# Performance work log

Hardware: AMD Instinct MI355X
Metric: run time of the kernel (lower is better)

The kernel has to match this reference:

```python
import jax, jax.numpy as jnp
import numpy as np

NUM_FEATURES = 602
NUM_CLASSES = 41
HIDDEN = 8
HEADS1 = 8
HEADS2 = 1
N_NODES = 100000
N_EDGES = 1600000
NEG_SLOPE = 0.2  # PyG GATConv default leaky_relu slope
EPS = 1e-16      # PyG softmax denominator epsilon


def gat_conv(x, edge_index, W, att_src, att_dst, bias, heads, out_ch, concat):
    """Faithful PyG GATConv forward (eval mode, dropout disabled).
    x: [N, F_in], edge_index: [2, E] with row0=src, row1=dst.
    W: [F_in, heads*out_ch], att_src/att_dst: [heads, out_ch], bias: [heads*out_ch] or [out_ch].
    """
    N = x.shape[0]
    h = (x @ W).reshape(N, heads, out_ch)              # [N, H, C]
    a_src = jnp.einsum('nhc,hc->nh', h, att_src)       # [N, H]
    a_dst = jnp.einsum('nhc,hc->nh', h, att_dst)       # [N, H]
    src, dst = edge_index[0], edge_index[1]
    e = jax.nn.leaky_relu(a_src[src] + a_dst[dst], NEG_SLOPE)  # [E, H]
    # segment softmax over incoming edges of each dst node
    m = jax.ops.segment_max(e, dst, num_segments=N)    # [N, H]
    e = jnp.exp(e - m[dst])
    denom = jax.ops.segment_sum(e, dst, num_segments=N)  # [N, H]
    alpha = e / (denom[dst] + EPS)                     # [E, H]
    msg = h[src] * alpha[:, :, None]                   # [E, H, C]
    out = jax.ops.segment_sum(msg, dst, num_segments=N)  # [N, H, C]
    if concat:
        out = out.reshape(N, heads * out_ch)
    else:
        out = out.mean(axis=1)
    return out + bias


def setup_inputs() -> dict:
    key = jax.random.key(0)
    ks = jax.random.split(key, 10)
    x = jax.random.normal(ks[0], (N_NODES, NUM_FEATURES), dtype=jnp.float32)
    edge_index = jax.random.randint(ks[1], (2, N_EDGES), 0, N_NODES, dtype=jnp.int64)
    s = 0.1
    W1 = jax.random.normal(ks[2], (NUM_FEATURES, HEADS1 * HIDDEN), dtype=jnp.float32) * s
    att_src1 = jax.random.normal(ks[3], (HEADS1, HIDDEN), dtype=jnp.float32) * s
    att_dst1 = jax.random.normal(ks[4], (HEADS1, HIDDEN), dtype=jnp.float32) * s
    b1 = jnp.zeros((HEADS1 * HIDDEN,), dtype=jnp.float32)
    W2 = jax.random.normal(ks[5], (HEADS1 * HIDDEN, HEADS2 * NUM_CLASSES), dtype=jnp.float32) * s
    att_src2 = jax.random.normal(ks[6], (HEADS2, NUM_CLASSES), dtype=jnp.float32) * s
    att_dst2 = jax.random.normal(ks[7], (HEADS2, NUM_CLASSES), dtype=jnp.float32) * s
    b2 = jnp.zeros((NUM_CLASSES,), dtype=jnp.float32)
    return {"x": x, "edge_index": edge_index, "W1": W1, "att_src1": att_src1,
            "att_dst1": att_dst1, "b1": b1, "W2": W2, "att_src2": att_src2,
            "att_dst2": att_dst2, "b2": b2}


def reference(x, edge_index, W1, att_src1, att_dst1, b1, W2, att_src2, att_dst2, b2):
    # eval mode: all F.dropout calls are identity
    h = gat_conv(x, edge_index, W1, att_src1, att_dst1, b1, HEADS1, HIDDEN, concat=True)
    h = jax.nn.elu(h)
    h = gat_conv(h, edge_index, W2, att_src2, att_dst2, b2, HEADS2, NUM_CLASSES, concat=False)
    return jax.nn.log_softmax(h, axis=1)
```

## Files before the change

kernel.cpp:

```cpp
#include <hip/hip_runtime.h>
#include <math.h>

#define NN 100000
#define NE 1600000
#define F_IN 602
#define H1 8
#define C1 8
#define F_MID 64
#define NC 41
#define NEG_SLOPE 0.2f
#define WT_LD 640

#define LRELU(x) fmaxf((x), NEG_SLOPE * (x))

typedef __attribute__((ext_vector_type(8))) short short8;
typedef __attribute__((ext_vector_type(4))) float f32x4;

__device__ inline unsigned short f2bf(float f) {
    unsigned u = __builtin_bit_cast(unsigned, f);
    unsigned r = (u + 0x7FFFu + ((u >> 16) & 1u)) >> 16;
    return (unsigned short)r;
}

__global__ void zero_kernel(int4* __restrict__ p, int n4)
{
    int i = blockIdx.x * blockDim.x + threadIdx.x;
    if (i < n4) p[i] = make_int4(0, 0, 0, 0);
}

__global__ void prep_wt_kernel(const float* __restrict__ W, unsigned short* __restrict__ Wt)
{
    int idx = blockIdx.x * blockDim.x + threadIdx.x;
    if (idx >= F_MID * WT_LD) return;
    int col = idx / WT_LD, k = idx % WT_LD;
    Wt[idx] = (k < F_IN) ? f2bf(W[k * F_MID + col]) : (unsigned short)0;
}

__global__ __launch_bounds__(256) void gemm1_mfma(
    const float* __restrict__ x, const unsigned short* __restrict__ Wt,
    float* __restrict__ h, int N)
{
    __shared__ unsigned short As[64][40];
    __shared__ unsigned short Bs[64][40];

    int t = threadIdx.x;
    int lane = t & 63;
    int w = t >> 6;
    int l16 = lane & 15, lg = lane >> 4;
    int n0 = blockIdx.x * 64;

    int arow = t >> 2, aseg = t & 3;
    int grow = n0 + arow;
    const float* xrow = x + (size_t)(grow < N ? grow : 0) * F_IN + aseg * 8;
    int bcol = t >> 2;
    const unsigned short* wrow = Wt + (size_t)bcol * WT_LD + aseg * 8;

    f32x4 acc[4] = {};
    float2 av[4];
    uint4  bv;

    #pragma unroll
    for (int i = 0; i < 4; ++i) av[i] = *(const float2*)(xrow + i * 2);
    bv = *(const uint4*)(wrow);

    for (int kt = 0; kt < 19; ++kt) {
        __syncthreads();
        {
            unsigned short tmp[8];
            #pragma unroll
            for (int i = 0; i < 4; ++i) {
                tmp[i * 2]     = f2bf(av[i].x);
                tmp[i * 2 + 1] = f2bf(av[i].y);
            }
            *(uint4*)(&As[arow][aseg * 8]) = *(uint4*)tmp;
            *(uint4*)(&Bs[bcol][aseg * 8]) = bv;
        }
        __syncthreads();

        if (kt < 18) {
            int k0 = (kt + 1) * 32;
            if (kt + 1 < 18) {
                #pragma unroll
                for (int i = 0; i < 4; ++i) av[i] = *(const float2*)(xrow + k0 + i * 2);
            } else {
                #pragma unroll
                for (int i = 0; i < 4; ++i) {
                    int k = k0 + aseg * 8 + i * 2;
                    float a = (k < F_IN)     ? xrow[k0 + i * 2]     : 0.f;
                    float b = (k + 1 < F_IN) ? xrow[k0 + i * 2 + 1] : 0.f;
                    av[i] = make_float2(a, b);
                }
            }
            bv = *(const uint4*)(wrow + k0);
        }

        short8 afrag = *(const short8*)(&As[w * 16 + l16][lg * 8]);
        short8 bfrag[4];
        #pragma unroll
        for (int n = 0; n < 4; ++n)
            bfrag[n] = *(const short8*)(&Bs[n * 16 + l16][lg * 8]);
        #pragma unroll
        for (int n = 0; n < 4; ++n)
            acc[n] = __builtin_amdgcn_mfma_f32_16x16x32_bf16(afrag, bfrag[n], acc[n], 0, 0, 0);
    }

    #pragma unroll
    for (int r = 0; r < 4; ++r) {
        int row = n0 + w * 16 + lg * 4 + r;
        if (row < N) {
            #pragma unroll
            for (int n = 0; n < 4; ++n)
                h[(size_t)row * F_MID + n * 16 + l16] = acc[n][r];
        }
    }
}

__global__ void attn1_kernel(const float* __restrict__ h,
                             const float* __restrict__ attS,
                             const float* __restrict__ attD,
                             float* __restrict__ asrc, float* __restrict__ adst, int N)
{
    int idx = blockIdx.x * blockDim.x + threadIdx.x;
    if (idx >= N * H1) return;
    int n = idx >> 3, hh = idx & 7;
    float s = 0.f, d = 0.f;
    #pragma unroll
    for (int c = 0; c < C1; ++c) {
        float v = h[n * F_MID + hh * C1 + c];
        s += v * attS[hh * C1 + c];
        d += v * attD[hh * C1 + c];
    }
    asrc[idx] = s;
    adst[idx] = d;
}

__global__ void deg_kernel(const int* __restrict__ dst, int* __restrict__ deg, int E)
{
    int e = blockIdx.x * blockDim.x + threadIdx.x;
    if (e < E) atomicAdd(&deg[dst[e]], 1);
}

__global__ void scan1_kernel(const int* __restrict__ deg, int* __restrict__ bsum, int N)
{
    int b = blockIdx.x, t = threadIdx.x;
    int base = b * 1024 + t * 16;
    int s = 0;
    #pragma unroll
    for (int i = 0; i < 16; ++i) { int idx = base + i; if (idx < N) s += deg[idx]; }
    #pragma unroll
    for (int o = 32; o > 0; o >>= 1) s += __shfl_down(s, o);
    if (t == 0) bsum[b] = s;
}

__global__ void scan2_kernel(const int* __restrict__ bsum, int* __restrict__ boff,
                             int nb, int* __restrict__ offs, int N, int E)
{
    __shared__ int buf[128];
    int t = threadIdx.x;
    int v = (t < nb) ? bsum[t] : 0;
    buf[t] = v;
    __syncthreads();
    for (int o = 1; o < 128; o <<= 1) {
        int u = (t >= o) ? buf[t - o] : 0;
        __syncthreads();
        buf[t] += u;
        __syncthreads();
    }
    if (t < nb) boff[t] = buf[t] - v;
    if (t == 0) offs[N] = E;
}

__global__ void scan3_kernel(const int* __restrict__ deg, const int* __restrict__ boff,
                             int* __restrict__ offs, int N)
{
    int b = blockIdx.x, t = threadIdx.x;
    int base = b * 1024 + t * 16;
    int loc[16];
    int s = 0;
    #pragma unroll
    for (int i = 0; i < 16; ++i) {
        int idx = base + i;
        loc[i] = (idx < N) ? deg[idx] : 0;
        s += loc[i];
    }
    int inc = s;
    #pragma unroll
    for (int o = 1; o < 64; o <<= 1) {
        int u = __shfl_up(inc, o);
        if (t >= o) inc += u;
    }
    int run = inc - s + boff[b];
    #pragma unroll
    for (int i = 0; i < 16; ++i) {
        int idx = base + i;
        if (idx < N) offs[idx] = run;
        run += loc[i];
    }
}

__global__ void scatter_kernel(const int* __restrict__ src, const int* __restrict__ dst,
                               const int* __restrict__ offs, int* __restrict__ cursor,
                               int* __restrict__ srcs, int E)
{
    int e = blockIdx.x * blockDim.x + threadIdx.x;
    if (e < E) {
        int d = dst[e];
        int pos = offs[d] + atomicAdd(&cursor[d], 1);
        srcs[pos] = src[e];
    }
}

__global__ void agg1_kernel(const int* __restrict__ offs, const int* __restrict__ srcs,
                            const float* __restrict__ h1,
                            const float* __restrict__ asrc, const float* __restrict__ adst,
                            const float* __restrict__ b1,
                            float* __restrict__ out1, int N)
{
    int wave = (blockIdx.x * blockDim.x + threadIdx.x) >> 6;
    int lane = threadIdx.x & 63;
    if (wave >= N) return;
    int n = wave;
    int hh = lane >> 3;
    int beg = offs[n], end = offs[n + 1];
    float ad = adst[n * H1 + hh];

    float m = -INFINITY, den = 0.f, acc = 0.f;
    int i = beg;
    for (; i + 4 <= end; i += 4) {
        int s0 = srcs[i], s1 = srcs[i + 1], s2 = srcs[i + 2], s3 = srcs[i + 3];
        float a0 = asrc[s0 * H1 + hh], a1 = asrc[s1 * H1 + hh];
        float a2 = asrc[s2 * H1 + hh], a3 = asrc[s3 * H1 + hh];
        float v0 = h1[s0 * F_MID + lane], v1 = h1[s1 * F_MID + lane];
        float v2 = h1[s2 * F_MID + lane], v3 = h1[s3 * F_MID + lane];
        float e0 = LRELU(a0 + ad), e1 = LRELU(a1 + ad);
        float e2 = LRELU(a2 + ad), e3 = LRELU(a3 + ad);
        float m4 = fmaxf(fmaxf(e0, e1), fmaxf(e2, e3));
        float mn = fmaxf(m, m4);
        float sc = __expf(m - mn);
        float p0 = __expf(e0 - mn), p1 = __expf(e1 - mn);
        float p2 = __expf(e2 - mn), p3 = __expf(e3 - mn);
        den = den * sc + ((p0 + p1) + (p2 + p3));
        acc = acc * sc + ((p0 * v0 + p1 * v1) + (p2 * v2 + p3 * v3));
        m = mn;
    }
    for (; i < end; ++i) {
        int s = srcs[i];
        float e = LRELU(asrc[s * H1 + hh] + ad);
        float hv = h1[s * F_MID + lane];
        float mn = fmaxf(m, e);
        float sc = __expf(m - mn);
        float p  = __expf(e - mn);
        den = den * sc + p;
        acc = acc * sc + p * hv;
        m = mn;
    }
    float inv = 1.f / (den + 1e-16f);
    float v = acc * inv + b1[lane];
    out1[n * F_MID + lane] = v > 0.f ? v : expm1f(v);
}

__global__ __launch_bounds__(256) void gemm2_kernel(
    const float* __restrict__ out1, const float* __restrict__ W2,
    float* __restrict__ h2, int N)
{
    __shared__ float ws[F_MID * NC];
    for (int i = threadIdx.x; i < F_MID * NC; i += 256) ws[i] = W2[i];
    __syncthreads();
    int idx = blockIdx.x * blockDim.x + threadIdx.x;
    if (idx >= N * NC) return;
    int n = idx / NC, j = idx % NC;
    const float* row = out1 + n * F_MID;
    float acc = 0.f;
    #pragma unroll
    for (int k = 0; k < F_MID; ++k) acc += row[k] * ws[k * NC + j];
    h2[idx] = acc;
}

__global__ void attn2_kernel(const float* __restrict__ h2,
                             const float* __restrict__ attS,
                             const float* __restrict__ attD,
                             float* __restrict__ asrc, float* __restrict__ adst, int N)
{
    int n = blockIdx.x * blockDim.x + threadIdx.x;
    if (n >= N) return;
    float s = 0.f, d = 0.f;
    #pragma unroll
    for (int j = 0; j < NC; ++j) {
        float v = h2[n * NC + j];
        s += v * attS[j];
        d += v * attD[j];
    }
    asrc[n] = s;
    adst[n] = d;
}

__global__ void agg2_kernel(const int* __restrict__ offs, const int* __restrict__ srcs,
                            const float* __restrict__ h2,
                            const float* __restrict__ asrc, const float* __restrict__ adst,
                            const float* __restrict__ b2,
                            float* __restrict__ out, int N)
{
    int wave = (blockIdx.x * blockDim.x + threadIdx.x) >> 6;
    int lane = threadIdx.x & 63;
    if (wave >= N) return;
    int n = wave;
    int beg = offs[n], end = offs[n + 1];
    float ad = adst[n];
    bool act = lane < NC;

    float m = -INFINITY, den = 0.f, acc = 0.f;
    int i = beg;
    for (; i + 4 <= end; i += 4) {
        int s0 = srcs[i], s1 = srcs[i + 1], s2 = srcs[i + 2], s3 = srcs[i + 3];
        float a0 = asrc[s0], a1 = asrc[s1], a2 = asrc[s2], a3 = asrc[s3];
        float v0 = act ? h2[s0 * NC + lane] : 0.f;
        float v1 = act ? h2[s1 * NC + lane] : 0.f;
        float v2 = act ? h2[s2 * NC + lane] : 0.f;
        float v3 = act ? h2[s3 * NC + lane] : 0.f;
        float e0 = LRELU(a0 + ad), e1 = LRELU(a1 + ad);
        float e2 = LRELU(a2 + ad), e3 = LRELU(a3 + ad);
        float m4 = fmaxf(fmaxf(e0, e1), fmaxf(e2, e3));
        float mn = fmaxf(m, m4);
        float sc = __expf(m - mn);
        float p0 = __expf(e0 - mn), p1 = __expf(e1 - mn);
        float p2 = __expf(e2 - mn), p3 = __expf(e3 - mn);
        den = den * sc + ((p0 + p1) + (p2 + p3));
        acc = acc * sc + ((p0 * v0 + p1 * v1) + (p2 * v2 + p3 * v3));
        m = mn;
    }
    for (; i < end; ++i) {
        int s = srcs[i];
        float e = LRELU(asrc[s] + ad);
        float hv = act ? h2[s * NC + lane] : 0.f;
        float mn = fmaxf(m, e);
        float sc = __expf(m - mn);
        float p  = __expf(e - mn);
        den = den * sc + p;
        acc = acc * sc + p * hv;
        m = mn;
    }
    float inv = 1.f / (den + 1e-16f);
    float v = act ? acc * inv + b2[lane] : -INFINITY;
    float mm = v;
    #pragma unroll
    for (int o = 32; o > 0; o >>= 1) mm = fmaxf(mm, __shfl_xor(mm, o));
    float ex = act ? __expf(v - mm) : 0.f;
    float S = ex;
    #pragma unroll
    for (int o = 32; o > 0; o >>= 1) S += __shfl_xor(S, o);
    if (act) out[n * NC + lane] = v - mm - logf(S);
}

extern "C" void kernel_launch(void* const* d_in, const int* in_sizes, int n_in,
                              void* d_out, int out_size, void* d_ws, size_t ws_size,
                              hipStream_t stream)
{
    const float* x     = (const float*)d_in[0];
    const int*   ei    = (const int*)  d_in[1];
    const float* W1    = (const float*)d_in[2];
    const float* attS1 = (const float*)d_in[3];
    const float* attD1 = (const float*)d_in[4];
    const float* b1    = (const float*)d_in[5];
    const float* W2    = (const float*)d_in[6];
    const float* attS2 = (const float*)d_in[7];
    const float* attD2 = (const float*)d_in[8];
    const float* b2    = (const float*)d_in[9];
    float* out = (float*)d_out;

    const int N = NN, E = NE;
    const int* src = ei;
    const int* dst = ei + E;

    char* p = (char*)d_ws;
    auto alloc = [&](size_t bytes) { char* r = p; p += (bytes + 255) & ~255ull; return r; };
    float* h1    = (float*)alloc((size_t)N * F_MID * 4);
    float* asrc1 = (float*)alloc((size_t)N * H1 * 4);
    float* adst1 = (float*)alloc((size_t)N * H1 * 4);
    float* out1  = (float*)alloc((size_t)N * F_MID * 4);
    float* h2    = (float*)alloc((size_t)N * NC * 4);
    float* asrc2 = (float*)alloc((size_t)N * 4);
    float* adst2 = (float*)alloc((size_t)N * 4);
    int*   deg   = (int*)alloc((size_t)2 * N * 4);
    int*   cursor= deg + N;
    int*   offs  = (int*)alloc((size_t)(N + 1) * 4);
    int*   srcs  = (int*)alloc((size_t)E * 4);
    unsigned short* Wt = (unsigned short*)alloc((size_t)F_MID * WT_LD * 2);
    const int NB = (N + 1023) / 1024;
    int*   bsum  = (int*)alloc((size_t)NB * 4);
    int*   boff  = (int*)alloc((size_t)NB * 4);

    const int n4 = (2 * N) / 4;
    zero_kernel<<<(n4 + 255) / 256, 256, 0, stream>>>((int4*)deg, n4);

    prep_wt_kernel<<<(F_MID * WT_LD + 255) / 256, 256, 0, stream>>>(W1, Wt);
    gemm1_mfma<<<(N + 63) / 64, 256, 0, stream>>>(x, Wt, h1, N);
    attn1_kernel<<<(N * H1 + 255) / 256, 256, 0, stream>>>(h1, attS1, attD1, asrc1, adst1, N);
    deg_kernel<<<(E + 255) / 256, 256, 0, stream>>>(dst, deg, E);
    scan1_kernel<<<NB, 64, 0, stream>>>(deg, bsum, N);
    scan2_kernel<<<1, 128, 0, stream>>>(bsum, boff, NB, offs, N, E);
    scan3_kernel<<<NB, 64, 0, stream>>>(deg, boff, offs, N);
    scatter_kernel<<<(E + 255) / 256, 256, 0, stream>>>(src, dst, offs, cursor, srcs, E);
    agg1_kernel<<<(N * 64 + 255) / 256, 256, 0, stream>>>(offs, srcs, h1, asrc1, adst1, b1, out1, N);
    gemm2_kernel<<<(N * NC + 255) / 256, 256, 0, stream>>>(out1, W2, h2, N);
    attn2_kernel<<<(N + 255) / 256, 256, 0, stream>>>(h2, attS2, attD2, asrc2, adst2, N);
    agg2_kernel<<<(N * 64 + 255) / 256, 256, 0, stream>>>(offs, srcs, h2, asrc2, adst2, b2, out, N);
}
```

Measured before the change: 470.3 us.

## Pad layer-2 features and pack source attention score into row; unroll aggregation by eight

Layer-2 features are stored with a padded 48-float row stride, and the per-node source attention score is written into column 41 of the same row. The aggregation kernel then reads the score and features in one gather and broadcasts the score with a wave shuffle, removing a separate dependent random load per edge. Both aggregation kernels unroll the edge loop from four to eight to keep more gathers in flight. The cost is extra register pressure and a slightly larger h2 buffer.

```diff
diff --git a/kernel.cpp b/kernel.cpp
--- a/kernel.cpp
+++ b/kernel.cpp
@@ -8,6 +8,7 @@
 #define C1 8
 #define F_MID 64
 #define NC 41
+#define H2_LD 48
 #define NEG_SLOPE 0.2f
 #define WT_LD 640
 
@@ -226,21 +227,28 @@
 
     float m = -INFINITY, den = 0.f, acc = 0.f;
     int i = beg;
-    for (; i + 4 <= end; i += 4) {
-        int s0 = srcs[i], s1 = srcs[i + 1], s2 = srcs[i + 2], s3 = srcs[i + 3];
-        float a0 = asrc[s0 * H1 + hh], a1 = asrc[s1 * H1 + hh];
-        float a2 = asrc[s2 * H1 + hh], a3 = asrc[s3 * H1 + hh];
-        float v0 = h1[s0 * F_MID + lane], v1 = h1[s1 * F_MID + lane];
-        float v2 = h1[s2 * F_MID + lane], v3 = h1[s3 * F_MID + lane];
-        float e0 = LRELU(a0 + ad), e1 = LRELU(a1 + ad);
-        float e2 = LRELU(a2 + ad), e3 = LRELU(a3 + ad);
-        float m4 = fmaxf(fmaxf(e0, e1), fmaxf(e2, e3));
-        float mn = fmaxf(m, m4);
+    for (; i + 8 <= end; i += 8) {
+        int s[8];
+        #pragma unroll
+        for (int j = 0; j < 8; ++j) s[j] = srcs[i + j];
+        float a[8], v[8];
+        #pragma unroll
+        for (int j = 0; j < 8; ++j) a[j] = asrc[s[j] * H1 + hh];
+        #pragma unroll
+        for (int j = 0; j < 8; ++j) v[j] = h1[s[j] * F_MID + lane];
+        float e[8];
+        #pragma unroll
+        for (int j = 0; j < 8; ++j) e[j] = LRELU(a[j] + ad);
+        float m8 = fmaxf(fmaxf(fmaxf(e[0], e[1]), fmaxf(e[2], e[3])),
+                         fmaxf(fmaxf(e[4], e[5]), fmaxf(e[6], e[7])));
+        float mn = fmaxf(m, m8);
         float sc = __expf(m - mn);
-        float p0 = __expf(e0 - mn), p1 = __expf(e1 - mn);
-        float p2 = __expf(e2 - mn), p3 = __expf(e3 - mn);
-        den = den * sc + ((p0 + p1) + (p2 + p3));
-        acc = acc * sc + ((p0 * v0 + p1 * v1) + (p2 * v2 + p3 * v3));
+        float p[8];
+        #pragma unroll
+        for (int j = 0; j < 8; ++j) p[j] = __expf(e[j] - mn);
+        den = den * sc + (((p[0] + p[1]) + (p[2] + p[3])) + ((p[4] + p[5]) + (p[6] + p[7])));
+        acc = acc * sc + (((p[0] * v[0] + p[1] * v[1]) + (p[2] * v[2] + p[3] * v[3]))
+                        + ((p[4] * v[4] + p[5] * v[5]) + (p[6] * v[6] + p[7] * v[7])));
         m = mn;
     }
     for (; i < end; ++i) {
@@ -261,7 +269,7 @@
 
 __global__ __launch_bounds__(256) void gemm2_kernel(
     const float* __restrict__ out1, const float* __restrict__ W2,
-    float* __restrict__ h2, int N)
+    float* __restrict__ h2p, int N)
 {
     __shared__ float ws[F_MID * NC];
     for (int i = threadIdx.x; i < F_MID * NC; i += 256) ws[i] = W2[i];
@@ -273,30 +281,30 @@
     float acc = 0.f;
     #pragma unroll
     for (int k = 0; k < F_MID; ++k) acc += row[k] * ws[k * NC + j];
-    h2[idx] = acc;
-}
-
-__global__ void attn2_kernel(const float* __restrict__ h2,
+    h2p[n * H2_LD + j] = acc;
+}
+
+__global__ void attn2_kernel(float* __restrict__ h2p,
                              const float* __restrict__ attS,
                              const float* __restrict__ attD,
-                             float* __restrict__ asrc, float* __restrict__ adst, int N)
+                             float* __restrict__ adst, int N)
 {
     int n = blockIdx.x * blockDim.x + threadIdx.x;
     if (n >= N) return;
     float s = 0.f, d = 0.f;
     #pragma unroll
     for (int j = 0; j < NC; ++j) {
-        float v = h2[n * NC + j];
+        float v = h2p[n * H2_LD + j];
         s += v * attS[j];
         d += v * attD[j];
     }
-    asrc[n] = s;
+    h2p[n * H2_LD + NC] = s;
     adst[n] = d;
 }
 
 __global__ void agg2_kernel(const int* __restrict__ offs, const int* __restrict__ srcs,
-                            const float* __restrict__ h2,
-                            const float* __restrict__ asrc, const float* __restrict__ adst,
+                            const float* __restrict__ h2p,
+                            const float* __restrict__ adst,
                             const float* __restrict__ b2,
                             float* __restrict__ out, int N)
 {
@@ -307,31 +315,40 @@
     int beg = offs[n], end = offs[n + 1];
     float ad = adst[n];
     bool act = lane < NC;
+    int li = act ? lane : NC;
 
     float m = -INFINITY, den = 0.f, acc = 0.f;
     int i = beg;
-    for (; i + 4 <= end; i += 4) {
-        int s0 = srcs[i], s1 = srcs[i + 1], s2 = srcs[i + 2], s3 = srcs[i + 3];
-        float a0 = asrc[s0], a1 = asrc[s1], a2 = asrc[s2], a3 = asrc[s3];
-        float v0 = act ? h2[s0 * NC + lane] : 0.f;
-        float v1 = act ? h2[s1 * NC + lane] : 0.f;
-        float v2 = act ? h2[s2 * NC + lane] : 0.f;
-        float v3 = act ? h2[s3 * NC + lane] : 0.f;
-        float e0 = LRELU(a0 + ad), e1 = LRELU(a1 + ad);
-        float e2 = LRELU(a2 + ad), e3 = LRELU(a3 + ad);
-        float m4 = fmaxf(fmaxf(e0, e1), fmaxf(e2, e3));
-        float mn = fmaxf(m, m4);
+    for (; i + 8 <= end; i += 8) {
+        int s[8];
+        #pragma unroll
+        for (int j = 0; j < 8; ++j) s[j] = srcs[i + j];
+        float hv[8];
+        #pragma unroll
+        for (int j = 0; j < 8; ++j) hv[j] = h2p[s[j] * H2_LD + li];
+        float a[8];
+        #pragma unroll
+        for (int j = 0; j < 8; ++j) a[j] = __shfl(hv[j], NC);
+        float e[8];
+        #pragma unroll
+        for (int j = 0; j < 8; ++j) e[j] = LRELU(a[j] + ad);
+        float m8 = fmaxf(fmaxf(fmaxf(e[0], e[1]), fmaxf(e[2], e[3])),
+                         fmaxf(fmaxf(e[4], e[5]), fmaxf(e[6], e[7])));
+        float mn = fmaxf(m, m8);
         float sc = __expf(m - mn);
-        float p0 = __expf(e0 - mn), p1 = __expf(e1 - mn);
-        float p2 = __expf(e2 - mn), p3 = __expf(e3 - mn);
-        den = den * sc + ((p0 + p1) + (p2 + p3));
-        acc = acc * sc + ((p0 * v0 + p1 * v1) + (p2 * v2 + p3 * v3));
+        float p[8];
+        #pragma unroll
+        for (int j = 0; j < 8; ++j) p[j] = __expf(e[j] - mn);
+        den = den * sc + (((p[0] + p[1]) + (p[2] + p[3])) + ((p[4] + p[5]) + (p[6] + p[7])));
+        acc = acc * sc + (((p[0] * hv[0] + p[1] * hv[1]) + (p[2] * hv[2] + p[3] * hv[3]))
+                        + ((p[4] * hv[4] + p[5] * hv[5]) + (p[6] * hv[6] + p[7] * hv[7])));
         m = mn;
     }
     for (; i < end; ++i) {
         int s = srcs[i];
-        float e = LRELU(asrc[s] + ad);
-        float hv = act ? h2[s * NC + lane] : 0.f;
+        float hv = h2p[s * H2_LD + li];
+        float a = __shfl(hv, NC);
+        float e = LRELU(a + ad);
         float mn = fmaxf(m, e);
         float sc = __expf(m - mn);
         float p  = __expf(e - mn);
@@ -377,8 +394,7 @@
     float* asrc1 = (float*)alloc((size_t)N * H1 * 4);
     float* adst1 = (float*)alloc((size_t)N * H1 * 4);
     float* out1  = (float*)alloc((size_t)N * F_MID * 4);
-    float* h2    = (float*)alloc((size_t)N * NC * 4);
-    float* asrc2 = (float*)alloc((size_t)N * 4);
+    float* h2p   = (float*)alloc((size_t)N * H2_LD * 4);
     float* adst2 = (float*)alloc((size_t)N * 4);
     int*   deg   = (int*)alloc((size_t)2 * N * 4);
     int*   cursor= deg + N;
@@ -401,7 +417,7 @@
     scan3_kernel<<<NB, 64, 0, stream>>>(deg, boff, offs, N);
     scatter_kernel<<<(E + 255) / 256, 256, 0, stream>>>(src, dst, offs, cursor, srcs, E);
     agg1_kernel<<<(N * 64 + 255) / 256, 256, 0, stream>>>(offs, srcs, h1, asrc1, adst1, b1, out1, N);
-    gemm2_kernel<<<(N * NC + 255) / 256, 256, 0, stream>>>(out1, W2, h2, N);
-    attn2_kernel<<<(N + 255) / 256, 256, 0, stream>>>(h2, attS2, attD2, asrc2, adst2, N);
-    agg2_kernel<<<(N * 64 + 255) / 256, 256, 0, stream>>>(offs, srcs, h2, asrc2, adst2, b2, out, N);
-}
+    gemm2_kernel<<<(N * NC + 255) / 256, 256, 0, stream>>>(out1, W2, h2p, N);
+    attn2_kernel<<<(N + 255) / 256, 256, 0, stream>>>(h2p, attS2, attD2, adst2, N);
+    agg2_kernel<<<(N * 64 + 255) / 256, 256, 0, stream>>>(offs, srcs, h2p, adst2, b2, out, N);
+}
```

Measured after the change: 475.2 us. About the same (+1.0%).
